# Kernel optimization log

Hardware: AMD Instinct MI355X
Metric: run time of the kernel (lower is better)

## Reference

```python
import jax, jax.numpy as jnp
import numpy as np

B, N = 32, 64
ATTR, STATE, REL, GDIM = 4, 8, 4, 32
NF = 128

def _ln(x, w, b, eps=1e-5):
    mu = jnp.mean(x, axis=-1, keepdims=True)
    var = jnp.mean((x - mu) ** 2, axis=-1, keepdims=True)
    return (x - mu) * jax.lax.rsqrt(var + eps) * w + b

def setup_inputs() -> dict:
    key = jax.random.key(0)
    ks = iter(jax.random.split(key, 32))
    d = {}
    d['attrs'] = jax.random.normal(next(ks), (B, N, ATTR), jnp.float32)
    d['states'] = jax.random.normal(next(ks), (B, N, STATE), jnp.float32)
    d['actions'] = jnp.zeros((B, N, 4), jnp.float32)  # action=False, unused
    d['rel_attrs'] = jax.random.normal(next(ks), (B, N, N, REL), jnp.float32)
    def w(shape):
        return jax.random.normal(next(ks), shape, jnp.float32) * 0.05
    d['oe_w0'] = w((NF, ATTR + STATE)); d['oe_b0'] = jnp.zeros((NF,), jnp.float32)
    d['oe_w1'] = w((NF, NF));            d['oe_b1'] = jnp.zeros((NF,), jnp.float32)
    d['re_w0'] = w((NF, STATE + REL + 2 * ATTR)); d['re_b0'] = jnp.zeros((NF,), jnp.float32)
    d['re_w1'] = w((NF, NF));            d['re_b1'] = jnp.zeros((NF,), jnp.float32)
    d['rp_w'] = w((NF, NF + 2 * NF));    d['rp_b'] = jnp.zeros((NF,), jnp.float32)
    d['rp_lnw'] = jnp.ones((NF,), jnp.float32); d['rp_lnb'] = jnp.zeros((NF,), jnp.float32)
    d['pp_w'] = w((NF, 2 * NF));         d['pp_b'] = jnp.zeros((NF,), jnp.float32)
    d['pp_lnw'] = jnp.ones((NF,), jnp.float32); d['pp_lnb'] = jnp.zeros((NF,), jnp.float32)
    d['pr_w0'] = w((NF, NF));            d['pr_b0'] = jnp.zeros((NF,), jnp.float32)
    d['pr_w1'] = w((GDIM, NF));          d['pr_b1'] = jnp.zeros((GDIM,), jnp.float32)
    d['pstep'] = 2
    return d

def reference(attrs, states, actions, rel_attrs,
              oe_w0, oe_b0, oe_w1, oe_b1,
              re_w0, re_b0, re_w1, re_b1,
              rp_w, rp_b, rp_lnw, rp_lnb,
              pp_w, pp_b, pp_lnw, pp_lnb,
              pr_w0, pr_b0, pr_w1, pr_b1, pstep):
    lin = lambda x, w, b: jnp.einsum('...i,oi->...o', x, w) + b
    # ---- encode nodes: [B,N,attr+state] -> [B,N,NF] (action=False) ----
    obj_in = jnp.concatenate([attrs, states], axis=2)
    obj_encode = jax.nn.relu(lin(jax.nn.relu(lin(obj_in, oe_w0, oe_b0)), oe_w1, oe_b1))
    # ---- encode edges over dense N x N pairs ----
    rel_states = states[:, :, None, :] - states[:, None, :, :]        # B,N,N,state
    recv_attr = jnp.broadcast_to(attrs[:, :, None, :], (attrs.shape[0], attrs.shape[1], attrs.shape[1], attrs.shape[2]))
    send_attr = jnp.broadcast_to(attrs[:, None, :, :], recv_attr.shape)
    rel_in = jnp.concatenate([rel_attrs, rel_states, recv_attr, send_attr], axis=3)
    rel_encode = jax.nn.relu(lin(jax.nn.relu(lin(rel_in, re_w0, re_b0)), re_w1, re_b1))  # B,N,N,NF
    # ---- propagation steps ----
    for _ in range(pstep):
        sh = rel_encode.shape[:3] + (obj_encode.shape[-1],)
        recv = jnp.broadcast_to(obj_encode[:, :, None, :], sh)
        send = jnp.broadcast_to(obj_encode[:, None, :, :], sh)
        rel_effect = jax.nn.relu(_ln(lin(jnp.concatenate([rel_encode, recv, send], axis=3), rp_w, rp_b), rp_lnw, rp_lnb))
        rel_agg = rel_effect.sum(axis=2)                               # B,N,NF
        obj_encode = jax.nn.relu(_ln(lin(jnp.concatenate([obj_encode, rel_agg], axis=2), pp_w, pp_b), pp_lnw, pp_lnb))
    # ---- predict + tanh (state_encoder has tanh=True) ----
    out = lin(jax.nn.relu(lin(obj_encode, pr_w0, pr_b0)), pr_w1, pr_b1)
    return jnp.tanh(out)
```

## Files before the change

kernel.cpp:

```cpp
#include <hip/hip_runtime.h>


#define ROWS 2048
typedef unsigned short u16;
typedef unsigned int u32;
typedef __attribute__((ext_vector_type(8))) short bf16x8;
typedef __attribute__((ext_vector_type(4))) short bf16x4;
typedef __attribute__((ext_vector_type(4))) float f32x4;

__device__ __forceinline__ float bsu(u16 u) { return __uint_as_float(((u32)u) << 16); }
__device__ __forceinline__ u16 f2b(float f) {
    u32 u = __float_as_uint(f);
    u32 r = (u + 0x7fffu + ((u >> 16) & 1u)) >> 16;
    return (u16)r;
}

__global__ __launch_bounds__(256)
void k_prep(const float* __restrict__ re_w1, const float* __restrict__ rp_w,
            const float* __restrict__ oe_w1, const float* __restrict__ pp_w,
            const float* __restrict__ pr_w0, const float* __restrict__ pr_w1,
            u16* __restrict__ re_w1b, u16* __restrict__ web,
            u16* __restrict__ oe_w1b, u16* __restrict__ wrecvb, u16* __restrict__ wsendb,
            u16* __restrict__ pp_wb, u16* __restrict__ pr_w0b, u16* __restrict__ pr_w1b)
{
    int idx = blockIdx.x * 256 + threadIdx.x;
    if (idx < 16384) { re_w1b[idx] = f2b(re_w1[idx]); return; }
    idx -= 16384;
    if (idx < 16384) { int r = idx >> 7, c = idx & 127;
        web[idx] = f2b(rp_w[r * 384 + c]); return; }
    idx -= 16384;
    if (idx < 16384) { oe_w1b[idx] = f2b(oe_w1[idx]); return; }
    idx -= 16384;
    if (idx < 16384) { int r = idx >> 7, c = idx & 127;
        wrecvb[idx] = f2b(rp_w[r * 384 + 128 + c]); return; }
    idx -= 16384;
    if (idx < 16384) { int r = idx >> 7, c = idx & 127;
        wsendb[idx] = f2b(rp_w[r * 384 + 256 + c]); return; }
    idx -= 16384;
    if (idx < 32768) { pp_wb[idx] = f2b(pp_w[idx]); return; }
    idx -= 32768;
    if (idx < 16384) { pr_w0b[idx] = f2b(pr_w0[idx]); return; }
    idx -= 16384;
    if (idx < 4096)  { pr_w1b[idx] = f2b(pr_w1[idx]); }
}

__global__ __launch_bounds__(256)
void k_node(const float* __restrict__ attrs, const float* __restrict__ states,
            const float* __restrict__ oe_w0, const float* __restrict__ oe_b0,
            const u16* __restrict__ oe_w1b, const float* __restrict__ oe_b1,
            const float* __restrict__ re_w0, const float* __restrict__ re_b0,
            const u16* __restrict__ wrecvb, const u16* __restrict__ wsendb,
            const float* __restrict__ rp_b,
            u16* __restrict__ objb, float* __restrict__ nr, float* __restrict__ ns,
            float* __restrict__ recvT, float* __restrict__ sendT)
{
    const int r0 = blockIdx.x * 16;
    const int t = threadIdx.x;
    __shared__ float xs[16][12];
    __shared__ float w0s[1536];
    __shared__ float rw0s[2560];
    __shared__ __align__(16) u16 hb[16 * 136];
    __shared__ __align__(16) u16 ob[16 * 136];

    if (t < 192) { int row = t / 12, c = t - row * 12;
        xs[row][c] = (c < 4) ? attrs[(r0 + row) * 4 + c] : states[(r0 + row) * 8 + (c - 4)]; }
    for (int i = t; i < 1536; i += 256) w0s[i] = oe_w0[i];
    for (int i = t; i < 2560; i += 256) rw0s[i] = re_w0[i];
    __syncthreads();

    for (int e = t; e < 2048; e += 256) {
        int row = e >> 7, o = e & 127;
        float h = oe_b0[o];
#pragma unroll
        for (int k = 0; k < 12; k++) h += w0s[o * 12 + k] * xs[row][k];
        hb[row * 136 + o] = f2b(fmaxf(h, 0.f));
        float s0 = 0.f, a0 = 0.f, a1 = 0.f;
#pragma unroll
        for (int k = 0; k < 8; k++) s0 += rw0s[o * 20 + 4 + k] * xs[row][4 + k];
#pragma unroll
        for (int k = 0; k < 4; k++) {
            a0 += rw0s[o * 20 + 12 + k] * xs[row][k];
            a1 += rw0s[o * 20 + 16 + k] * xs[row][k];
        }
        nr[(r0 + row) * 128 + o] = s0 + a0 + re_b0[o];
        ns[(r0 + row) * 128 + o] = a1 - s0;
    }
    __syncthreads();

    const int wave = t >> 6, lane = t & 63, tx = lane & 15, quad = lane >> 4;

    bf16x8 afr[4];
#pragma unroll
    for (int kk = 0; kk < 4; kk++) afr[kk] = *(const bf16x8*)&hb[tx * 136 + kk * 32 + quad * 8];
    f32x4 acc[2]; acc[0] = (f32x4){0.f,0.f,0.f,0.f}; acc[1] = acc[0];
#pragma unroll
    for (int ot = 0; ot < 2; ot++) {
        int o = (wave * 2 + ot) * 16 + tx;
#pragma unroll
        for (int kk = 0; kk < 4; kk++) {
            bf16x8 bfr = *(const bf16x8*)&oe_w1b[o * 128 + kk * 32 + quad * 8];
            acc[ot] = __builtin_amdgcn_mfma_f32_16x16x32_bf16(afr[kk], bfr, acc[ot], 0, 0, 0);
        }
    }
#pragma unroll
    for (int ot = 0; ot < 2; ot++) {
        int o = (wave * 2 + ot) * 16 + tx;
        float bia = oe_b1[o];
#pragma unroll
        for (int r = 0; r < 4; r++)
            ob[(quad * 4 + r) * 136 + o] = f2b(fmaxf(acc[ot][r] + bia, 0.f));
    }
    __syncthreads();
    { int m = t >> 4, c = t & 15;
      *(uint4*)&objb[(r0 + m) * 128 + c * 8] = *(const uint4*)&ob[m * 136 + c * 8]; }

#pragma unroll
    for (int kk = 0; kk < 4; kk++) afr[kk] = *(const bf16x8*)&ob[tx * 136 + kk * 32 + quad * 8];
    f32x4 ar[2], an[2];
    ar[0] = (f32x4){0.f,0.f,0.f,0.f}; ar[1] = ar[0]; an[0] = ar[0]; an[1] = ar[0];
#pragma unroll
    for (int ot = 0; ot < 2; ot++) {
        int o = (wave * 2 + ot) * 16 + tx;
#pragma unroll
        for (int kk = 0; kk < 4; kk++) {
            bf16x8 br = *(const bf16x8*)&wrecvb[o * 128 + kk * 32 + quad * 8];
            ar[ot] = __builtin_amdgcn_mfma_f32_16x16x32_bf16(afr[kk], br, ar[ot], 0, 0, 0);
            bf16x8 bs = *(const bf16x8*)&wsendb[o * 128 + kk * 32 + quad * 8];
            an[ot] = __builtin_amdgcn_mfma_f32_16x16x32_bf16(afr[kk], bs, an[ot], 0, 0, 0);
        }
    }
#pragma unroll
    for (int ot = 0; ot < 2; ot++) {
        int o = (wave * 2 + ot) * 16 + tx;
        float rb = rp_b[o];
#pragma unroll
        for (int r = 0; r < 4; r++) {
            recvT[(r0 + quad * 4 + r) * 128 + o] = ar[ot][r] + rb;
            sendT[(r0 + quad * 4 + r) * 128 + o] = an[ot][r];
        }
    }
}

__global__ __launch_bounds__(256)
void k_edge_fused(const float* __restrict__ rel_attrs,
                  const float* __restrict__ re_w0, const u16* __restrict__ re_w1b,
                  const u16* __restrict__ web, const float* __restrict__ re_b1,
                  const float* __restrict__ rp_lnw, const float* __restrict__ rp_lnb,
                  const float* __restrict__ nr, const float* __restrict__ ns,
                  const float* __restrict__ recvT, const float* __restrict__ sendT,
                  u16* __restrict__ Ebuf, u16* __restrict__ aggb)
{
    const int blkg = blockIdx.x;
    const int b = blkg >> 6;
    const int t = threadIdx.x;
    __shared__ __align__(16) u16 hsb[64 * 144];
    __shared__ float nrs[128];
    __shared__ float w0a[128][4];
    __shared__ float ras[64][4];
    __shared__ float lnws[128], lnbs[128];
    __shared__ float redS[256], redQ[256];

    if (t < 128) {
        lnws[t] = rp_lnw[t]; lnbs[t] = rp_lnb[t];
        nrs[t] = nr[blkg * 128 + t];
#pragma unroll
        for (int c = 0; c < 4; c++) w0a[t][c] = re_w0[t * 20 + c];
    } else if (t < 192) {
        int j = t - 128;
#pragma unroll
        for (int c = 0; c < 4; c++) ras[j][c] = rel_attrs[(blkg * 64 + j) * 4 + c];
    }
    __syncthreads();

    const int w = t >> 6, lane = t & 63, tx = lane & 15, quad = lane >> 4;
    const int ob = w * 32;

    for (int e = t; e < 64 * 128; e += 256) {
        int j = e >> 7, o = e & 127;
        float v = nrs[o] + ns[(b * 64 + j) * 128 + o];
#pragma unroll
        for (int c = 0; c < 4; c++) v += w0a[o][c] * ras[j][c];
        hsb[j * 144 + o] = f2b(fmaxf(v, 0.f));
    }

    bf16x8 b1[2][4];
#pragma unroll
    for (int ot = 0; ot < 2; ot++)
#pragma unroll
        for (int kk = 0; kk < 4; kk++)
            b1[ot][kk] = *(const bf16x8*)&re_w1b[(ob + ot * 16 + tx) * 128 + kk * 32 + quad * 8];
    __syncthreads();

    f32x4 acc[4][2];
#pragma unroll
    for (int jt = 0; jt < 4; jt++) { acc[jt][0] = (f32x4){0.f,0.f,0.f,0.f}; acc[jt][1] = acc[jt][0]; }
#pragma unroll
    for (int jt = 0; jt < 4; jt++) {
        bf16x8 afr[4];
#pragma unroll
        for (int kk = 0; kk < 4; kk++)
            afr[kk] = *(const bf16x8*)&hsb[(jt * 16 + tx) * 144 + kk * 32 + quad * 8];
#pragma unroll
        for (int ot = 0; ot < 2; ot++)
#pragma unroll
            for (int kk = 0; kk < 4; kk++)
                acc[jt][ot] = __builtin_amdgcn_mfma_f32_16x16x32_bf16(afr[kk], b1[ot][kk], acc[jt][ot], 0, 0, 0);
    }
    __syncthreads();

    {
        float bia0 = re_b1[ob + tx], bia1 = re_b1[ob + 16 + tx];
#pragma unroll
        for (int jt = 0; jt < 4; jt++)
#pragma unroll
            for (int r = 0; r < 4; r++) {
                int j = jt * 16 + quad * 4 + r;
                hsb[j * 144 + ob + tx]      = f2b(fmaxf(acc[jt][0][r] + bia0, 0.f));
                hsb[j * 144 + ob + 16 + tx] = f2b(fmaxf(acc[jt][1][r] + bia1, 0.f));
            }
    }
    bf16x8 b2[2][4];
#pragma unroll
    for (int ot = 0; ot < 2; ot++)
#pragma unroll
        for (int kk = 0; kk < 4; kk++)
            b2[ot][kk] = *(const bf16x8*)&web[(ob + ot * 16 + tx) * 128 + kk * 32 + quad * 8];
    __syncthreads();

    f32x4 acc2[4][2];
#pragma unroll
    for (int jt = 0; jt < 4; jt++) { acc2[jt][0] = (f32x4){0.f,0.f,0.f,0.f}; acc2[jt][1] = acc2[jt][0]; }
#pragma unroll
    for (int jt = 0; jt < 4; jt++) {
        bf16x8 afr[4];
#pragma unroll
        for (int kk = 0; kk < 4; kk++)
            afr[kk] = *(const bf16x8*)&hsb[(jt * 16 + tx) * 144 + kk * 32 + quad * 8];
#pragma unroll
        for (int ot = 0; ot < 2; ot++)
#pragma unroll
            for (int kk = 0; kk < 4; kk++)
                acc2[jt][ot] = __builtin_amdgcn_mfma_f32_16x16x32_bf16(afr[kk], b2[ot][kk], acc2[jt][ot], 0, 0, 0);
    }

#pragma unroll
    for (int jt = 0; jt < 4; jt++)
#pragma unroll
        for (int ot = 0; ot < 2; ot++) {
            bf16x4 v;
            v[0] = (short)f2b(acc2[jt][ot][0]); v[1] = (short)f2b(acc2[jt][ot][1]);
            v[2] = (short)f2b(acc2[jt][ot][2]); v[3] = (short)f2b(acc2[jt][ot][3]);
            *(bf16x4*)(Ebuf + ((size_t)((blkg * 4 + jt) * 8 + (2 * w + ot)) * 64 + lane) * 4) = v;
        }

    {
        float rv0 = recvT[blkg * 128 + ob + tx];
        float rv1 = recvT[blkg * 128 + ob + 16 + tx];
#pragma unroll
        for (int jt = 0; jt < 4; jt++)
#pragma unroll
            for (int r = 0; r < 4; r++) {
                int j = b * 64 + jt * 16 + quad * 4 + r;
                acc2[jt][0][r] += rv0 + sendT[j * 128 + ob + tx];
                acc2[jt][1][r] += rv1 + sendT[j * 128 + ob + 16 + tx];
            }
    }

#pragma unroll
    for (int jt = 0; jt < 4; jt++) {
        float s4[4], q4[4];
#pragma unroll
        for (int r = 0; r < 4; r++) {
            float a0 = acc2[jt][0][r], a1 = acc2[jt][1][r];
            s4[r] = a0 + a1; q4[r] = a0 * a0 + a1 * a1;
        }
#pragma unroll
        for (int m = 1; m < 16; m <<= 1)
#pragma unroll
            for (int r = 0; r < 4; r++) {
                s4[r] += __shfl_xor(s4[r], m, 64);
                q4[r] += __shfl_xor(q4[r], m, 64);
            }
        if (tx == 0)
#pragma unroll
            for (int r = 0; r < 4; r++) {
                redS[w * 64 + jt * 16 + quad * 4 + r] = s4[r];
                redQ[w * 64 + jt * 16 + quad * 4 + r] = q4[r];
            }
    }
    __syncthreads();

    {
        float lw0 = lnws[ob + tx], lb0 = lnbs[ob + tx];
        float lw1 = lnws[ob + 16 + tx], lb1 = lnbs[ob + 16 + tx];
        float ag0 = 0.f, ag1 = 0.f;
#pragma unroll
        for (int jt = 0; jt < 4; jt++)
#pragma unroll
            for (int r = 0; r < 4; r++) {
                int row = jt * 16 + quad * 4 + r;
                float ss = redS[row] + redS[64 + row] + redS[128 + row] + redS[192 + row];
                float qq = redQ[row] + redQ[64 + row] + redQ[128 + row] + redQ[192 + row];
                float mu = ss * (1.f / 128.f);
                float rsd = rsqrtf(qq * (1.f / 128.f) - mu * mu + 1e-5f);
                float z0 = (acc2[jt][0][r] - mu) * rsd * lw0 + lb0;
                float z1 = (acc2[jt][1][r] - mu) * rsd * lw1 + lb1;
                ag0 += fmaxf(z0, 0.f);
                ag1 += fmaxf(z1, 0.f);
            }
        ag0 += __shfl_xor(ag0, 16, 64); ag0 += __shfl_xor(ag0, 32, 64);
        ag1 += __shfl_xor(ag1, 16, 64); ag1 += __shfl_xor(ag1, 32, 64);
        if (quad == 0) {
            aggb[blkg * 128 + ob + tx]      = f2b(ag0);
            aggb[blkg * 128 + ob + 16 + tx] = f2b(ag1);
        }
    }
}

__global__ __launch_bounds__(256)
void k_prop_edge2(const u16* __restrict__ Ebuf,
                  const float* __restrict__ rp_lnw, const float* __restrict__ rp_lnb,
                  const float* __restrict__ recvT, const float* __restrict__ sendT,
                  u16* __restrict__ aggb)
{
    const int blk = blockIdx.x;
    const int b = blk >> 6;
    const int t = threadIdx.x;
    __shared__ float scr[16 * 132];
    __shared__ float lnws[128], lnbs[128];
    if (t < 128) { lnws[t] = rp_lnw[t]; lnbs[t] = rp_lnb[t]; }
    __syncthreads();

    const int wave = t >> 6, lane = t & 63, tx = lane & 15, quad = lane >> 4;
    const int tid = blk * 4 + wave;
    const int jrow = wave * 16 + quad * 4;

    float y[8][4];
#pragma unroll
    for (int oo = 0; oo < 8; oo++) {
        bf16x4 v = *(const bf16x4*)(Ebuf + ((size_t)(tid * 8 + oo) * 64 + lane) * 4);
        const int o = oo * 16 + tx;
        float rv = recvT[blk * 128 + o];
#pragma unroll
        for (int r = 0; r < 4; r++)
            y[oo][r] = bsu((u16)v[r]) + rv + sendT[(b * 64 + jrow + r) * 128 + o];
    }
    float s[4], q[4];
#pragma unroll
    for (int r = 0; r < 4; r++) {
        s[r] = 0.f; q[r] = 0.f;
#pragma unroll
        for (int oo = 0; oo < 8; oo++) { s[r] += y[oo][r]; q[r] += y[oo][r] * y[oo][r]; }
    }
#pragma unroll
    for (int m = 1; m < 16; m <<= 1) {
#pragma unroll
        for (int r = 0; r < 4; r++) {
            s[r] += __shfl_xor(s[r], m, 64);
            q[r] += __shfl_xor(q[r], m, 64);
        }
    }
    float mu[4], rs[4];
#pragma unroll
    for (int r = 0; r < 4; r++) {
        mu[r] = s[r] * (1.f / 128.f);
        rs[r] = rsqrtf(q[r] * (1.f / 128.f) - mu[r] * mu[r] + 1e-5f);
    }
    float pa[8];
#pragma unroll
    for (int oo = 0; oo < 8; oo++) {
        const int o = oo * 16 + tx;
        float lw = lnws[o], lb = lnbs[o];
        float p = 0.f;
#pragma unroll
        for (int r = 0; r < 4; r++) {
            float z = (y[oo][r] - mu[r]) * rs[r] * lw + lb;
            p += fmaxf(z, 0.f);
        }
        pa[oo] = p;
    }
    const int grp = wave * 4 + quad;
#pragma unroll
    for (int oo = 0; oo < 8; oo++) scr[grp * 132 + oo * 16 + tx] = pa[oo];
    __syncthreads();
    if (t < 128) {
        float sum = 0.f;
#pragma unroll
        for (int gg = 0; gg < 16; gg++) sum += scr[gg * 132 + t];
        aggb[blk * 128 + t] = f2b(sum);
    }
}

__global__ __launch_bounds__(256)
void k_prop_node(const u16* __restrict__ aggb,
                 const u16* __restrict__ pp_wb, const float* __restrict__ pp_b,
                 const float* __restrict__ pp_lnw, const float* __restrict__ pp_lnb,
                 const u16* __restrict__ wrecvb, const u16* __restrict__ wsendb,
                 const float* __restrict__ rp_b,
                 u16* __restrict__ objb, float* __restrict__ recvT, float* __restrict__ sendT,
                 int compute_terms)
{
    const int r0 = blockIdx.x * 16;
    const int t = threadIdx.x;
    __shared__ __align__(16) u16 ab[16 * 264];
    __shared__ __align__(16) u16 ob[16 * 136];
    __shared__ float redS[64], redQ[64];

    for (int i = t; i < 512; i += 256) {
        int m = i >> 5, c = i & 31;
        uint4 v = (c < 16) ? *(const uint4*)&objb[(r0 + m) * 128 + (c & 15) * 8]
                           : *(const uint4*)&aggb[(r0 + m) * 128 + (c - 16) * 8];
        *(uint4*)&ab[m * 264 + c * 8] = v;
    }
    __syncthreads();

    const int wave = t >> 6, lane = t & 63, tx = lane & 15, quad = lane >> 4;
    bf16x8 afr[8];
#pragma unroll
    for (int kk = 0; kk < 8; kk++) afr[kk] = *(const bf16x8*)&ab[tx * 264 + kk * 32 + quad * 8];
    f32x4 acc[2]; acc[0] = (f32x4){0.f,0.f,0.f,0.f}; acc[1] = acc[0];
#pragma unroll
    for (int ot = 0; ot < 2; ot++) {
        int o = (wave * 2 + ot) * 16 + tx;
#pragma unroll
        for (int kk = 0; kk < 8; kk++) {
            bf16x8 bfr = *(const bf16x8*)&pp_wb[o * 256 + kk * 32 + quad * 8];
            acc[ot] = __builtin_amdgcn_mfma_f32_16x16x32_bf16(afr[kk], bfr, acc[ot], 0, 0, 0);
        }
    }
#pragma unroll
    for (int ot = 0; ot < 2; ot++) {
        float bia = pp_b[(wave * 2 + ot) * 16 + tx];
#pragma unroll
        for (int r = 0; r < 4; r++) acc[ot][r] += bia;
    }

    float s[4], q[4];
#pragma unroll
    for (int r = 0; r < 4; r++) {
        s[r] = acc[0][r] + acc[1][r];
        q[r] = acc[0][r] * acc[0][r] + acc[1][r] * acc[1][r];
    }
#pragma unroll
    for (int m = 1; m < 16; m <<= 1) {
#pragma unroll
        for (int r = 0; r < 4; r++) {
            s[r] += __shfl_xor(s[r], m, 64);
            q[r] += __shfl_xor(q[r], m, 64);
        }
    }
    if (tx == 0) {
#pragma unroll
        for (int r = 0; r < 4; r++) {
            redS[wave * 16 + quad * 4 + r] = s[r];
            redQ[wave * 16 + quad * 4 + r] = q[r];
        }
    }
    __syncthreads();
    float mu[4], rs[4];
#pragma unroll
    for (int r = 0; r < 4; r++) {
        int m = quad * 4 + r;
        float ss = redS[m] + redS[16 + m] + redS[32 + m] + redS[48 + m];
        float qq = redQ[m] + redQ[16 + m] + redQ[32 + m] + redQ[48 + m];
        mu[r] = ss * (1.f / 128.f);
        rs[r] = rsqrtf(qq * (1.f / 128.f) - mu[r] * mu[r] + 1e-5f);
    }
#pragma unroll
    for (int ot = 0; ot < 2; ot++) {
        int o = (wave * 2 + ot) * 16 + tx;
        float lw = pp_lnw[o], lb = pp_lnb[o];
#pragma unroll
        for (int r = 0; r < 4; r++) {
            float z = (acc[ot][r] - mu[r]) * rs[r] * lw + lb;
            ob[(quad * 4 + r) * 136 + o] = f2b(fmaxf(z, 0.f));
        }
    }
    __syncthreads();
    { int m = t >> 4, c = t & 15;
      *(uint4*)&objb[(r0 + m) * 128 + c * 8] = *(const uint4*)&ob[m * 136 + c * 8]; }

    if (compute_terms) {
        bf16x8 af2[4];
#pragma unroll
        for (int kk = 0; kk < 4; kk++) af2[kk] = *(const bf16x8*)&ob[tx * 136 + kk * 32 + quad * 8];
        f32x4 ar[2], an[2];
        ar[0] = (f32x4){0.f,0.f,0.f,0.f}; ar[1] = ar[0]; an[0] = ar[0]; an[1] = ar[0];
#pragma unroll
        for (int ot = 0; ot < 2; ot++) {
            int o = (wave * 2 + ot) * 16 + tx;
#pragma unroll
            for (int kk = 0; kk < 4; kk++) {
                bf16x8 br = *(const bf16x8*)&wrecvb[o * 128 + kk * 32 + quad * 8];
                ar[ot] = __builtin_amdgcn_mfma_f32_16x16x32_bf16(af2[kk], br, ar[ot], 0, 0, 0);
                bf16x8 bs = *(const bf16x8*)&wsendb[o * 128 + kk * 32 + quad * 8];
                an[ot] = __builtin_amdgcn_mfma_f32_16x16x32_bf16(af2[kk], bs, an[ot], 0, 0, 0);
            }
        }
#pragma unroll
        for (int ot = 0; ot < 2; ot++) {
            int o = (wave * 2 + ot) * 16 + tx;
            float rb = rp_b[o];
#pragma unroll
            for (int r = 0; r < 4; r++) {
                recvT[(r0 + quad * 4 + r) * 128 + o] = ar[ot][r] + rb;
                sendT[(r0 + quad * 4 + r) * 128 + o] = an[ot][r];
            }
        }
    }
}

__global__ __launch_bounds__(256)
void k_predict(const u16* __restrict__ objb,
               const u16* __restrict__ pr_w0b, const float* __restrict__ pr_b0,
               const u16* __restrict__ pr_w1b, const float* __restrict__ pr_b1,
               float* __restrict__ out)
{
    const int r0 = blockIdx.x * 16;
    const int t = threadIdx.x;
    __shared__ __align__(16) u16 ab[16 * 136];
    __shared__ __align__(16) u16 hb2[16 * 136];
    { int m = t >> 4, c = t & 15;
      *(uint4*)&ab[m * 136 + c * 8] = *(const uint4*)&objb[(r0 + m) * 128 + c * 8]; }
    __syncthreads();

    const int wave = t >> 6, lane = t & 63, tx = lane & 15, quad = lane >> 4;
    bf16x8 afr[4];
#pragma unroll
    for (int kk = 0; kk < 4; kk++) afr[kk] = *(const bf16x8*)&ab[tx * 136 + kk * 32 + quad * 8];
    f32x4 acc[2]; acc[0] = (f32x4){0.f,0.f,0.f,0.f}; acc[1] = acc[0];
#pragma unroll
    for (int ot = 0; ot < 2; ot++) {
        int o = (wave * 2 + ot) * 16 + tx;
#pragma unroll
        for (int kk = 0; kk < 4; kk++) {
            bf16x8 bfr = *(const bf16x8*)&pr_w0b[o * 128 + kk * 32 + quad * 8];
            acc[ot] = __builtin_amdgcn_mfma_f32_16x16x32_bf16(afr[kk], bfr, acc[ot], 0, 0, 0);
        }
    }
#pragma unroll
    for (int ot = 0; ot < 2; ot++) {
        int o = (wave * 2 + ot) * 16 + tx;
        float bia = pr_b0[o];
#pragma unroll
        for (int r = 0; r < 4; r++)
            hb2[(quad * 4 + r) * 136 + o] = f2b(fmaxf(acc[ot][r] + bia, 0.f));
    }
    __syncthreads();
    if (wave < 2) {
        bf16x8 af2[4];
#pragma unroll
        for (int kk = 0; kk < 4; kk++) af2[kk] = *(const bf16x8*)&hb2[tx * 136 + kk * 32 + quad * 8];
        f32x4 a2 = (f32x4){0.f,0.f,0.f,0.f};
        int o = wave * 16 + tx;
#pragma unroll
        for (int kk = 0; kk < 4; kk++) {
            bf16x8 bfr = *(const bf16x8*)&pr_w1b[o * 128 + kk * 32 + quad * 8];
            a2 = __builtin_amdgcn_mfma_f32_16x16x32_bf16(af2[kk], bfr, a2, 0, 0, 0);
        }
        float bia = pr_b1[o];
#pragma unroll
        for (int r = 0; r < 4; r++)
            out[(r0 + quad * 4 + r) * 32 + o] = tanhf(a2[r] + bia);
    }
}

extern "C" void kernel_launch(void* const* d_in, const int* in_sizes, int n_in,
                              void* d_out, int out_size, void* d_ws, size_t ws_size,
                              hipStream_t stream)
{
    const float* attrs    = (const float*)d_in[0];
    const float* states   = (const float*)d_in[1];
    const float* rel_attrs= (const float*)d_in[3];
    const float* oe_w0 = (const float*)d_in[4];
    const float* oe_b0 = (const float*)d_in[5];
    const float* oe_w1 = (const float*)d_in[6];
    const float* oe_b1 = (const float*)d_in[7];
    const float* re_w0 = (const float*)d_in[8];
    const float* re_b0 = (const float*)d_in[9];
    const float* re_w1 = (const float*)d_in[10];
    const float* re_b1 = (const float*)d_in[11];
    const float* rp_w  = (const float*)d_in[12];
    const float* rp_b  = (const float*)d_in[13];
    const float* rp_lnw= (const float*)d_in[14];
    const float* rp_lnb= (const float*)d_in[15];
    const float* pp_w  = (const float*)d_in[16];
    const float* pp_b  = (const float*)d_in[17];
    const float* pp_lnw= (const float*)d_in[18];
    const float* pp_lnb= (const float*)d_in[19];
    const float* pr_w0 = (const float*)d_in[20];
    const float* pr_b0 = (const float*)d_in[21];
    const float* pr_w1 = (const float*)d_in[22];
    const float* pr_b1 = (const float*)d_in[23];

    float* ws    = (float*)d_ws;
    float* nr    = ws;
    float* ns    = nr    + ROWS * 128;
    float* recvT = ns    + ROWS * 128;
    float* sendT = recvT + ROWS * 128;
    u16* re_w1b = (u16*)(sendT + ROWS * 128);
    u16* web    = re_w1b + 16384;
    u16* oe_w1b = web    + 16384;
    u16* wrecvb = oe_w1b + 16384;
    u16* wsendb = wrecvb + 16384;
    u16* pp_wb  = wsendb + 16384;
    u16* pr_w0b = pp_wb  + 32768;
    u16* pr_w1b = pr_w0b + 16384;
    u16* objb   = pr_w1b + 4096;
    u16* aggb   = objb + ROWS * 128;
    u16* Ebuf   = aggb + ROWS * 128;

    k_prep<<<528, 256, 0, stream>>>(re_w1, rp_w, oe_w1, pp_w, pr_w0, pr_w1,
                                    re_w1b, web, oe_w1b, wrecvb, wsendb,
                                    pp_wb, pr_w0b, pr_w1b);
    k_node<<<128, 256, 0, stream>>>(attrs, states, oe_w0, oe_b0, oe_w1b, oe_b1,
                                    re_w0, re_b0, wrecvb, wsendb, rp_b,
                                    objb, nr, ns, recvT, sendT);
    k_edge_fused<<<2048, 256, 0, stream>>>(rel_attrs, re_w0, re_w1b, web, re_b1,
                                           rp_lnw, rp_lnb, nr, ns, recvT, sendT,
                                           Ebuf, aggb);
    k_prop_node<<<128, 256, 0, stream>>>(aggb, pp_wb, pp_b, pp_lnw, pp_lnb,
                                         wrecvb, wsendb, rp_b,
                                         objb, recvT, sendT, 1);
    k_prop_edge2<<<2048, 256, 0, stream>>>(Ebuf, rp_lnw, rp_lnb, recvT, sendT, aggb);
    k_prop_node<<<128, 256, 0, stream>>>(aggb, pp_wb, pp_b, pp_lnw, pp_lnb,
                                         wrecvb, wsendb, rp_b,
                                         objb, recvT, sendT, 0);
    k_predict<<<128, 256, 0, stream>>>(objb, pr_w0b, pr_b0, pr_w1b, pr_b1, (float*)d_out);
}
```

Before: 187.4 us.

## Fold weight prep into node kernel and fuse final prop-node with predict

Removes the separate weight-conversion kernel. Its bf16 conversion now runs in a grid-stride loop inside the node kernel, which also reads fp32 weights directly and converts them in registers. The last propagation node step and the predict MLP are merged into one kernel. The edge kernel's first-layer setup is vectorised with float4 loads and packed bf16 stores, without the shared-memory staging. The aim is fewer kernel launches and fewer sync points, at the cost of extra work and register pressure in the node kernel.

```diff
diff --git a/kernel.cpp b/kernel.cpp
--- a/kernel.cpp
+++ b/kernel.cpp
@@ -1,11 +1,11 @@
 #include <hip/hip_runtime.h>
+#include <hip/hip_bf16.h>
 
 
 #define ROWS 2048
 typedef unsigned short u16;
 typedef unsigned int u32;
 typedef __attribute__((ext_vector_type(8))) short bf16x8;
-typedef __attribute__((ext_vector_type(4))) short bf16x4;
 typedef __attribute__((ext_vector_type(4))) float f32x4;
 
 __device__ __forceinline__ float bsu(u16 u) { return __uint_as_float(((u32)u) << 16); }
@@ -14,43 +14,30 @@
     u32 r = (u + 0x7fffu + ((u >> 16) & 1u)) >> 16;
     return (u16)r;
 }
-
-__global__ __launch_bounds__(256)
-void k_prep(const float* __restrict__ re_w1, const float* __restrict__ rp_w,
-            const float* __restrict__ oe_w1, const float* __restrict__ pp_w,
-            const float* __restrict__ pr_w0, const float* __restrict__ pr_w1,
-            u16* __restrict__ re_w1b, u16* __restrict__ web,
-            u16* __restrict__ oe_w1b, u16* __restrict__ wrecvb, u16* __restrict__ wsendb,
-            u16* __restrict__ pp_wb, u16* __restrict__ pr_w0b, u16* __restrict__ pr_w1b)
-{
-    int idx = blockIdx.x * 256 + threadIdx.x;
-    if (idx < 16384) { re_w1b[idx] = f2b(re_w1[idx]); return; }
-    idx -= 16384;
-    if (idx < 16384) { int r = idx >> 7, c = idx & 127;
-        web[idx] = f2b(rp_w[r * 384 + c]); return; }
-    idx -= 16384;
-    if (idx < 16384) { oe_w1b[idx] = f2b(oe_w1[idx]); return; }
-    idx -= 16384;
-    if (idx < 16384) { int r = idx >> 7, c = idx & 127;
-        wrecvb[idx] = f2b(rp_w[r * 384 + 128 + c]); return; }
-    idx -= 16384;
-    if (idx < 16384) { int r = idx >> 7, c = idx & 127;
-        wsendb[idx] = f2b(rp_w[r * 384 + 256 + c]); return; }
-    idx -= 16384;
-    if (idx < 32768) { pp_wb[idx] = f2b(pp_w[idx]); return; }
-    idx -= 32768;
-    if (idx < 16384) { pr_w0b[idx] = f2b(pr_w0[idx]); return; }
-    idx -= 16384;
-    if (idx < 4096)  { pr_w1b[idx] = f2b(pr_w1[idx]); }
+__device__ __forceinline__ u32 pk2(float a, float b) {
+    __hip_bfloat162 h = __float22bfloat162_rn(float2{a, b});
+    union { __hip_bfloat162 h; u32 u; } c; c.h = h; return c.u;
+}
+__device__ __forceinline__ bf16x8 ldcvt8(const float* __restrict__ p) {
+    float4 a = *(const float4*)p;
+    float4 b = *(const float4*)(p + 4);
+    union { u32 u[4]; bf16x8 v; } x;
+    x.u[0] = pk2(a.x, a.y); x.u[1] = pk2(a.z, a.w);
+    x.u[2] = pk2(b.x, b.y); x.u[3] = pk2(b.z, b.w);
+    return x.v;
 }
 
 __global__ __launch_bounds__(256)
 void k_node(const float* __restrict__ attrs, const float* __restrict__ states,
             const float* __restrict__ oe_w0, const float* __restrict__ oe_b0,
-            const u16* __restrict__ oe_w1b, const float* __restrict__ oe_b1,
+            const float* __restrict__ oe_w1, const float* __restrict__ oe_b1,
             const float* __restrict__ re_w0, const float* __restrict__ re_b0,
-            const u16* __restrict__ wrecvb, const u16* __restrict__ wsendb,
-            const float* __restrict__ rp_b,
+            const float* __restrict__ rp_w,  const float* __restrict__ rp_b,
+            const float* __restrict__ re_w1, const float* __restrict__ pp_w,
+            const float* __restrict__ pr_w0, const float* __restrict__ pr_w1,
+            u16* __restrict__ re_w1b, u16* __restrict__ web, u16* __restrict__ pp_wb,
+            u16* __restrict__ wrecvb, u16* __restrict__ wsendb,
+            u16* __restrict__ pr_w0b, u16* __restrict__ pr_w1b,
             u16* __restrict__ objb, float* __restrict__ nr, float* __restrict__ ns,
             float* __restrict__ recvT, float* __restrict__ sendT)
 {
@@ -62,6 +49,26 @@
     __shared__ __align__(16) u16 hb[16 * 136];
     __shared__ __align__(16) u16 ob[16 * 136];
 
+    {
+        int gid = blockIdx.x * 256 + t;
+        for (int i = gid; i < 118784; i += 32768) {
+            int idx = i;
+            if (idx < 16384) { re_w1b[idx] = f2b(re_w1[idx]); continue; }
+            idx -= 16384;
+            if (idx < 16384) { web[idx] = f2b(rp_w[(idx >> 7) * 384 + (idx & 127)]); continue; }
+            idx -= 16384;
+            if (idx < 32768) { pp_wb[idx] = f2b(pp_w[idx]); continue; }
+            idx -= 32768;
+            if (idx < 16384) { wrecvb[idx] = f2b(rp_w[(idx >> 7) * 384 + 128 + (idx & 127)]); continue; }
+            idx -= 16384;
+            if (idx < 16384) { wsendb[idx] = f2b(rp_w[(idx >> 7) * 384 + 256 + (idx & 127)]); continue; }
+            idx -= 16384;
+            if (idx < 16384) { pr_w0b[idx] = f2b(pr_w0[idx]); continue; }
+            idx -= 16384;
+            pr_w1b[idx] = f2b(pr_w1[idx]);
+        }
+    }
+
     if (t < 192) { int row = t / 12, c = t - row * 12;
         xs[row][c] = (c < 4) ? attrs[(r0 + row) * 4 + c] : states[(r0 + row) * 8 + (c - 4)]; }
     for (int i = t; i < 1536; i += 256) w0s[i] = oe_w0[i];
@@ -98,7 +105,7 @@
         int o = (wave * 2 + ot) * 16 + tx;
 #pragma unroll
         for (int kk = 0; kk < 4; kk++) {
-            bf16x8 bfr = *(const bf16x8*)&oe_w1b[o * 128 + kk * 32 + quad * 8];
+            bf16x8 bfr = ldcvt8(&oe_w1[o * 128 + kk * 32 + quad * 8]);
             acc[ot] = __builtin_amdgcn_mfma_f32_16x16x32_bf16(afr[kk], bfr, acc[ot], 0, 0, 0);
         }
     }
@@ -123,9 +130,9 @@
         int o = (wave * 2 + ot) * 16 + tx;
 #pragma unroll
         for (int kk = 0; kk < 4; kk++) {
-            bf16x8 br = *(const bf16x8*)&wrecvb[o * 128 + kk * 32 + quad * 8];
+            bf16x8 br = ldcvt8(&rp_w[o * 384 + 128 + kk * 32 + quad * 8]);
             ar[ot] = __builtin_amdgcn_mfma_f32_16x16x32_bf16(afr[kk], br, ar[ot], 0, 0, 0);
-            bf16x8 bs = *(const bf16x8*)&wsendb[o * 128 + kk * 32 + quad * 8];
+            bf16x8 bs = ldcvt8(&rp_w[o * 384 + 256 + kk * 32 + quad * 8]);
             an[ot] = __builtin_amdgcn_mfma_f32_16x16x32_bf16(afr[kk], bs, an[ot], 0, 0, 0);
         }
     }
@@ -154,34 +161,43 @@
     const int b = blkg >> 6;
     const int t = threadIdx.x;
     __shared__ __align__(16) u16 hsb[64 * 144];
-    __shared__ float nrs[128];
-    __shared__ float w0a[128][4];
-    __shared__ float ras[64][4];
     __shared__ float lnws[128], lnbs[128];
     __shared__ float redS[256], redQ[256];
 
-    if (t < 128) {
-        lnws[t] = rp_lnw[t]; lnbs[t] = rp_lnb[t];
-        nrs[t] = nr[blkg * 128 + t];
-#pragma unroll
-        for (int c = 0; c < 4; c++) w0a[t][c] = re_w0[t * 20 + c];
-    } else if (t < 192) {
-        int j = t - 128;
-#pragma unroll
-        for (int c = 0; c < 4; c++) ras[j][c] = rel_attrs[(blkg * 64 + j) * 4 + c];
-    }
-    __syncthreads();
+    if (t < 128) { lnws[t] = rp_lnw[t]; lnbs[t] = rp_lnb[t]; }
+
+    {
+        const int o0 = (t & 15) * 8;
+        const int jb = t >> 4;
+        float4 nr0 = *(const float4*)&nr[blkg * 128 + o0];
+        float4 nr1 = *(const float4*)&nr[blkg * 128 + o0 + 4];
+        float4 wreg[8];
+#pragma unroll
+        for (int k = 0; k < 8; k++) wreg[k] = *(const float4*)&re_w0[(o0 + k) * 20];
+#pragma unroll
+        for (int it = 0; it < 4; it++) {
+            int j = jb + it * 16;
+            float4 ra = *(const float4*)&rel_attrs[((size_t)blkg * 64 + j) * 4];
+            const float* nsp = &ns[(b * 64 + j) * 128 + o0];
+            float4 na = *(const float4*)nsp;
+            float4 nb = *(const float4*)(nsp + 4);
+            float v[8];
+            v[0] = nr0.x + na.x; v[1] = nr0.y + na.y; v[2] = nr0.z + na.z; v[3] = nr0.w + na.w;
+            v[4] = nr1.x + nb.x; v[5] = nr1.y + nb.y; v[6] = nr1.z + nb.z; v[7] = nr1.w + nb.w;
+#pragma unroll
+            for (int k = 0; k < 8; k++) {
+                v[k] += wreg[k].x * ra.x + wreg[k].y * ra.y + wreg[k].z * ra.z + wreg[k].w * ra.w;
+                v[k] = fmaxf(v[k], 0.f);
+            }
+            union { u32 u[4]; uint4 q; } p;
+            p.u[0] = pk2(v[0], v[1]); p.u[1] = pk2(v[2], v[3]);
+            p.u[2] = pk2(v[4], v[5]); p.u[3] = pk2(v[6], v[7]);
+            *(uint4*)&hsb[j * 144 + o0] = p.q;
+        }
+    }
 
     const int w = t >> 6, lane = t & 63, tx = lane & 15, quad = lane >> 4;
     const int ob = w * 32;
-
-    for (int e = t; e < 64 * 128; e += 256) {
-        int j = e >> 7, o = e & 127;
-        float v = nrs[o] + ns[(b * 64 + j) * 128 + o];
-#pragma unroll
-        for (int c = 0; c < 4; c++) v += w0a[o][c] * ras[j][c];
-        hsb[j * 144 + o] = f2b(fmaxf(v, 0.f));
-    }
 
     bf16x8 b1[2][4];
 #pragma unroll
@@ -247,10 +263,10 @@
     for (int jt = 0; jt < 4; jt++)
 #pragma unroll
         for (int ot = 0; ot < 2; ot++) {
-            bf16x4 v;
-            v[0] = (short)f2b(acc2[jt][ot][0]); v[1] = (short)f2b(acc2[jt][ot][1]);
-            v[2] = (short)f2b(acc2[jt][ot][2]); v[3] = (short)f2b(acc2[jt][ot][3]);
-            *(bf16x4*)(Ebuf + ((size_t)((blkg * 4 + jt) * 8 + (2 * w + ot)) * 64 + lane) * 4) = v;
+            uint2 ev;
+            ev.x = pk2(acc2[jt][ot][0], acc2[jt][ot][1]);
+            ev.y = pk2(acc2[jt][ot][2], acc2[jt][ot][3]);
+            *(uint2*)(Ebuf + ((size_t)((blkg * 4 + jt) * 8 + (2 * w + ot)) * 64 + lane) * 4) = ev;
         }
 
     {
@@ -338,12 +354,15 @@
     float y[8][4];
 #pragma unroll
     for (int oo = 0; oo < 8; oo++) {
-        bf16x4 v = *(const bf16x4*)(Ebuf + ((size_t)(tid * 8 + oo) * 64 + lane) * 4);
+        uint2 ev = *(const uint2*)(Ebuf + ((size_t)(tid * 8 + oo) * 64 + lane) * 4);
         const int o = oo * 16 + tx;
         float rv = recvT[blk * 128 + o];
-#pragma unroll
-        for (int r = 0; r < 4; r++)
-            y[oo][r] = bsu((u16)v[r]) + rv + sendT[(b * 64 + jrow + r) * 128 + o];
+        float e0 = bsu((u16)(ev.x & 0xffff)), e1 = bsu((u16)(ev.x >> 16));
+        float e2 = bsu((u16)(ev.y & 0xffff)), e3 = bsu((u16)(ev.y >> 16));
+        y[oo][0] = e0 + rv + sendT[(b * 64 + jrow + 0) * 128 + o];
+        y[oo][1] = e1 + rv + sendT[(b * 64 + jrow + 1) * 128 + o];
+        y[oo][2] = e2 + rv + sendT[(b * 64 + jrow + 2) * 128 + o];
+        y[oo][3] = e3 + rv + sendT[(b * 64 + jrow + 3) * 128 + o];
     }
     float s[4], q[4];
 #pragma unroll
@@ -392,13 +411,12 @@
 }
 
 __global__ __launch_bounds__(256)
-void k_prop_node(const u16* __restrict__ aggb,
-                 const u16* __restrict__ pp_wb, const float* __restrict__ pp_b,
-                 const float* __restrict__ pp_lnw, const float* __restrict__ pp_lnb,
-                 const u16* __restrict__ wrecvb, const u16* __restrict__ wsendb,
-                 const float* __restrict__ rp_b,
-                 u16* __restrict__ objb, float* __restrict__ recvT, float* __restrict__ sendT,
-                 int compute_terms)
+void k_pn0(const u16* __restrict__ aggb,
+           const u16* __restrict__ pp_wb, const float* __restrict__ pp_b,
+           const float* __restrict__ pp_lnw, const float* __restrict__ pp_lnb,
+           const u16* __restrict__ wrecvb, const u16* __restrict__ wsendb,
+           const float* __restrict__ rp_b,
+           u16* __restrict__ objb, float* __restrict__ recvT, float* __restrict__ sendT)
 {
     const int r0 = blockIdx.x * 16;
     const int t = threadIdx.x;
@@ -480,62 +498,133 @@
     { int m = t >> 4, c = t & 15;
       *(uint4*)&objb[(r0 + m) * 128 + c * 8] = *(const uint4*)&ob[m * 136 + c * 8]; }
 
-    if (compute_terms) {
-        bf16x8 af2[4];
-#pragma unroll
-        for (int kk = 0; kk < 4; kk++) af2[kk] = *(const bf16x8*)&ob[tx * 136 + kk * 32 + quad * 8];
-        f32x4 ar[2], an[2];
-        ar[0] = (f32x4){0.f,0.f,0.f,0.f}; ar[1] = ar[0]; an[0] = ar[0]; an[1] = ar[0];
-#pragma unroll
-        for (int ot = 0; ot < 2; ot++) {
-            int o = (wave * 2 + ot) * 16 + tx;
-#pragma unroll
-            for (int kk = 0; kk < 4; kk++) {
-                bf16x8 br = *(const bf16x8*)&wrecvb[o * 128 + kk * 32 + quad * 8];
-                ar[ot] = __builtin_amdgcn_mfma_f32_16x16x32_bf16(af2[kk], br, ar[ot], 0, 0, 0);
-                bf16x8 bs = *(const bf16x8*)&wsendb[o * 128 + kk * 32 + quad * 8];
-                an[ot] = __builtin_amdgcn_mfma_f32_16x16x32_bf16(af2[kk], bs, an[ot], 0, 0, 0);
-            }
-        }
-#pragma unroll
-        for (int ot = 0; ot < 2; ot++) {
-            int o = (wave * 2 + ot) * 16 + tx;
-            float rb = rp_b[o];
-#pragma unroll
-            for (int r = 0; r < 4; r++) {
-                recvT[(r0 + quad * 4 + r) * 128 + o] = ar[ot][r] + rb;
-                sendT[(r0 + quad * 4 + r) * 128 + o] = an[ot][r];
-            }
+    bf16x8 af2[4];
+#pragma unroll
+    for (int kk = 0; kk < 4; kk++) af2[kk] = *(const bf16x8*)&ob[tx * 136 + kk * 32 + quad * 8];
+    f32x4 ar[2], an[2];
+    ar[0] = (f32x4){0.f,0.f,0.f,0.f}; ar[1] = ar[0]; an[0] = ar[0]; an[1] = ar[0];
+#pragma unroll
+    for (int ot = 0; ot < 2; ot++) {
+        int o = (wave * 2 + ot) * 16 + tx;
+#pragma unroll
+        for (int kk = 0; kk < 4; kk++) {
+            bf16x8 br = *(const bf16x8*)&wrecvb[o * 128 + kk * 32 + quad * 8];
+            ar[ot] = __builtin_amdgcn_mfma_f32_16x16x32_bf16(af2[kk], br, ar[ot], 0, 0, 0);
+            bf16x8 bs = *(const bf16x8*)&wsendb[o * 128 + kk * 32 + quad * 8];
+            an[ot] = __builtin_amdgcn_mfma_f32_16x16x32_bf16(af2[kk], bs, an[ot], 0, 0, 0);
+        }
+    }
+#pragma unroll
+    for (int ot = 0; ot < 2; ot++) {
+        int o = (wave * 2 + ot) * 16 + tx;
+        float rb = rp_b[o];
+#pragma unroll
+        for (int r = 0; r < 4; r++) {
+            recvT[(r0 + quad * 4 + r) * 128 + o] = ar[ot][r] + rb;
+            sendT[(r0 + quad * 4 + r) * 128 + o] = an[ot][r];
         }
     }
 }
 
 __global__ __launch_bounds__(256)
-void k_predict(const u16* __restrict__ objb,
+void k_pn1pred(const u16* __restrict__ aggb,
+               const u16* __restrict__ pp_wb, const float* __restrict__ pp_b,
+               const float* __restrict__ pp_lnw, const float* __restrict__ pp_lnb,
+               const u16* __restrict__ objb,
                const u16* __restrict__ pr_w0b, const float* __restrict__ pr_b0,
                const u16* __restrict__ pr_w1b, const float* __restrict__ pr_b1,
                float* __restrict__ out)
 {
     const int r0 = blockIdx.x * 16;
     const int t = threadIdx.x;
-    __shared__ __align__(16) u16 ab[16 * 136];
+    __shared__ __align__(16) u16 ab[16 * 264];
+    __shared__ __align__(16) u16 ob[16 * 136];
     __shared__ __align__(16) u16 hb2[16 * 136];
-    { int m = t >> 4, c = t & 15;
-      *(uint4*)&ab[m * 136 + c * 8] = *(const uint4*)&objb[(r0 + m) * 128 + c * 8]; }
+    __shared__ float redS[64], redQ[64];
+
+    for (int i = t; i < 512; i += 256) {
+        int m = i >> 5, c = i & 31;
+        uint4 v = (c < 16) ? *(const uint4*)&objb[(r0 + m) * 128 + (c & 15) * 8]
+                           : *(const uint4*)&aggb[(r0 + m) * 128 + (c - 16) * 8];
+        *(uint4*)&ab[m * 264 + c * 8] = v;
+    }
     __syncthreads();
 
     const int wave = t >> 6, lane = t & 63, tx = lane & 15, quad = lane >> 4;
-    bf16x8 afr[4];
-#pragma unroll
-    for (int kk = 0; kk < 4; kk++) afr[kk] = *(const bf16x8*)&ab[tx * 136 + kk * 32 + quad * 8];
+    bf16x8 afr[8];
+#pragma unroll
+    for (int kk = 0; kk < 8; kk++) afr[kk] = *(const bf16x8*)&ab[tx * 264 + kk * 32 + quad * 8];
     f32x4 acc[2]; acc[0] = (f32x4){0.f,0.f,0.f,0.f}; acc[1] = acc[0];
+#pragma unroll
+    for (int ot = 0; ot < 2; ot++) {
+        int o = (wave * 2 + ot) * 16 + tx;
+#pragma unroll
+        for (int kk = 0; kk < 8; kk++) {
+            bf16x8 bfr = *(const bf16x8*)&pp_wb[o * 256 + kk * 32 + quad * 8];
+            acc[ot] = __builtin_amdgcn_mfma_f32_16x16x32_bf16(afr[kk], bfr, acc[ot], 0, 0, 0);
+        }
+    }
+#pragma unroll
+    for (int ot = 0; ot < 2; ot++) {
+        float bia = pp_b[(wave * 2 + ot) * 16 + tx];
+#pragma unroll
+        for (int r = 0; r < 4; r++) acc[ot][r] += bia;
+    }
+
+    float s[4], q[4];
+#pragma unroll
+    for (int r = 0; r < 4; r++) {
+        s[r] = acc[0][r] + acc[1][r];
+        q[r] = acc[0][r] * acc[0][r] + acc[1][r] * acc[1][r];
+    }
+#pragma unroll
+    for (int m = 1; m < 16; m <<= 1) {
+#pragma unroll
+        for (int r = 0; r < 4; r++) {
+            s[r] += __shfl_xor(s[r], m, 64);
+            q[r] += __shfl_xor(q[r], m, 64);
+        }
+    }
+    if (tx == 0) {
+#pragma unroll
+        for (int r = 0; r < 4; r++) {
+            redS[wave * 16 + quad * 4 + r] = s[r];
+            redQ[wave * 16 + quad * 4 + r] = q[r];
+        }
+    }
+    __syncthreads();
+    float mu[4], rs[4];
+#pragma unroll
+    for (int r = 0; r < 4; r++) {
+        int m = quad * 4 + r;
+        float ss = redS[m] + redS[16 + m] + redS[32 + m] + redS[48 + m];
+        float qq = redQ[m] + redQ[16 + m] + redQ[32 + m] + redQ[48 + m];
+        mu[r] = ss * (1.f / 128.f);
+        rs[r] = rsqrtf(qq * (1.f / 128.f) - mu[r] * mu[r] + 1e-5f);
+    }
+#pragma unroll
+    for (int ot = 0; ot < 2; ot++) {
+        int o = (wave * 2 + ot) * 16 + tx;
+        float lw = pp_lnw[o], lb = pp_lnb[o];
+#pragma unroll
+        for (int r = 0; r < 4; r++) {
+            float z = (acc[ot][r] - mu[r]) * rs[r] * lw + lb;
+            ob[(quad * 4 + r) * 136 + o] = f2b(fmaxf(z, 0.f));
+        }
+    }
+    __syncthreads();
+
+    bf16x8 af2[4];
+#pragma unroll
+    for (int kk = 0; kk < 4; kk++) af2[kk] = *(const bf16x8*)&ob[tx * 136 + kk * 32 + quad * 8];
+    f32x4 ah[2]; ah[0] = (f32x4){0.f,0.f,0.f,0.f}; ah[1] = ah[0];
 #pragma unroll
     for (int ot = 0; ot < 2; ot++) {
         int o = (wave * 2 + ot) * 16 + tx;
 #pragma unroll
         for (int kk = 0; kk < 4; kk++) {
             bf16x8 bfr = *(const bf16x8*)&pr_w0b[o * 128 + kk * 32 + quad * 8];
-            acc[ot] = __builtin_amdgcn_mfma_f32_16x16x32_bf16(afr[kk], bfr, acc[ot], 0, 0, 0);
+            ah[ot] = __builtin_amdgcn_mfma_f32_16x16x32_bf16(af2[kk], bfr, ah[ot], 0, 0, 0);
         }
     }
 #pragma unroll
@@ -544,19 +633,20 @@
         float bia = pr_b0[o];
 #pragma unroll
         for (int r = 0; r < 4; r++)
-            hb2[(quad * 4 + r) * 136 + o] = f2b(fmaxf(acc[ot][r] + bia, 0.f));
-    }
-    __syncthreads();
+            hb2[(quad * 4 + r) * 136 + o] = f2b(fmaxf(ah[ot][r] + bia, 0.f));
+    }
+    __syncthreads();
+
     if (wave < 2) {
-        bf16x8 af2[4];
-#pragma unroll
-        for (int kk = 0; kk < 4; kk++) af2[kk] = *(const bf16x8*)&hb2[tx * 136 + kk * 32 + quad * 8];
+        bf16x8 af3[4];
+#pragma unroll
+        for (int kk = 0; kk < 4; kk++) af3[kk] = *(const bf16x8*)&hb2[tx * 136 + kk * 32 + quad * 8];
         f32x4 a2 = (f32x4){0.f,0.f,0.f,0.f};
         int o = wave * 16 + tx;
 #pragma unroll
         for (int kk = 0; kk < 4; kk++) {
             bf16x8 bfr = *(const bf16x8*)&pr_w1b[o * 128 + kk * 32 + quad * 8];
-            a2 = __builtin_amdgcn_mfma_f32_16x16x32_bf16(af2[kk], bfr, a2, 0, 0, 0);
+            a2 = __builtin_amdgcn_mfma_f32_16x16x32_bf16(af3[kk], bfr, a2, 0, 0, 0);
         }
         float bia = pr_b1[o];
 #pragma unroll
@@ -600,31 +690,26 @@
     float* sendT = recvT + ROWS * 128;
     u16* re_w1b = (u16*)(sendT + ROWS * 128);
     u16* web    = re_w1b + 16384;
-    u16* oe_w1b = web    + 16384;
-    u16* wrecvb = oe_w1b + 16384;
+    u16* pp_wb  = web    + 16384;
+    u16* wrecvb = pp_wb  + 32768;
     u16* wsendb = wrecvb + 16384;
-    u16* pp_wb  = wsendb + 16384;
-    u16* pr_w0b = pp_wb  + 32768;
+    u16* pr_w0b = wsendb + 16384;
     u16* pr_w1b = pr_w0b + 16384;
     u16* objb   = pr_w1b + 4096;
     u16* aggb   = objb + ROWS * 128;
     u16* Ebuf   = aggb + ROWS * 128;
 
-    k_prep<<<528, 256, 0, stream>>>(re_w1, rp_w, oe_w1, pp_w, pr_w0, pr_w1,
-                                    re_w1b, web, oe_w1b, wrecvb, wsendb,
-                                    pp_wb, pr_w0b, pr_w1b);
-    k_node<<<128, 256, 0, stream>>>(attrs, states, oe_w0, oe_b0, oe_w1b, oe_b1,
-                                    re_w0, re_b0, wrecvb, wsendb, rp_b,
+    k_node<<<128, 256, 0, stream>>>(attrs, states, oe_w0, oe_b0, oe_w1, oe_b1,
+                                    re_w0, re_b0, rp_w, rp_b,
+                                    re_w1, pp_w, pr_w0, pr_w1,
+                                    re_w1b, web, pp_wb, wrecvb, wsendb, pr_w0b, pr_w1b,
                                     objb, nr, ns, recvT, sendT);
     k_edge_fused<<<2048, 256, 0, stream>>>(rel_attrs, re_w0, re_w1b, web, re_b1,
                                            rp_lnw, rp_lnb, nr, ns, recvT, sendT,
                                            Ebuf, aggb);
-    k_prop_node<<<128, 256, 0, stream>>>(aggb, pp_wb, pp_b, pp_lnw, pp_lnb,
-                                         wrecvb, wsendb, rp_b,
-                                         objb, recvT, sendT, 1);
+    k_pn0<<<128, 256, 0, stream>>>(aggb, pp_wb, pp_b, pp_lnw, pp_lnb,
+                                   wrecvb, wsendb, rp_b, objb, recvT, sendT);
     k_prop_edge2<<<2048, 256, 0, stream>>>(Ebuf, rp_lnw, rp_lnb, recvT, sendT, aggb);
-    k_prop_node<<<128, 256, 0, stream>>>(aggb, pp_wb, pp_b, pp_lnw, pp_lnb,
-                                         wrecvb, wsendb, rp_b,
-                                         objb, recvT, sendT, 0);
-    k_predict<<<128, 256, 0, stream>>>(objb, pr_w0b, pr_b0, pr_w1b, pr_b1, (float*)d_out);
-}
+    k_pn1pred<<<128, 256, 0, stream>>>(aggb, pp_wb, pp_b, pp_lnw, pp_lnb, objb,
+                                       pr_w0b, pr_b0, pr_w1b, pr_b1, (float*)d_out);
+}
```

After: 190.1 us. About the same (+1.4%).
